# Kernel tuning notes

Hardware: AMD Instinct MI355X
Metric: run time of the kernel (lower is better)

## Reference

```python
import jax, jax.numpy as jnp
import numpy as np

CLAMP = 6.0  # clamp_delta


def _causal_dw_conv(x, w, b):
    # x: [B, D, L], w: [D, W] depthwise taps, b: [D]; torch Conv1d(groups=D, padding=W-1)[..., :L]
    W = w.shape[1]
    L = x.shape[-1]
    xp = jnp.pad(x, ((0, 0), (0, 0), (W - 1, 0)))
    y = b[None, :, None]
    for i in range(W):  # small fixed kernel width (2 or 4)
        y = y + xp[:, :, i:i + L] * w[:, i][None, :, None]
    return y


def _selective_scan(u, delta, A, Bm, Cm, D, z, delta_bias):
    # u, delta: [B, Di, L]; A: [Di, N]; Bm, Cm: [B, N, L]; D, delta_bias: [Di]; z: [B, Di, L]
    d = jax.nn.softplus(delta + delta_bias[None, :, None])

    def step(s, inp):
        d_t, b_t, c_t, u_t = inp  # [B,Di], [B,N], [B,N], [B,Di]
        s = s * jnp.exp(d_t[..., None] * A) + (d_t * u_t)[..., None] * b_t[:, None, :]
        return s, jnp.einsum('bdn,bn->bd', s, c_t)

    s0 = jnp.zeros((u.shape[0], A.shape[0], A.shape[1]), u.dtype)
    xs = (d.transpose(2, 0, 1), Bm.transpose(2, 0, 1), Cm.transpose(2, 0, 1), u.transpose(2, 0, 1))
    _, ys = jax.lax.scan(step, s0, xs)  # ys: [L, B, Di]
    y = ys.transpose(1, 2, 0) + D[:, None] * u
    return y * jax.nn.silu(z)


def _mamba(h, in_w, conv_w, conv_b, xproj_w, dt_w, dt_b, A_log, D, out_w):
    # standard Mamba block (no fast path), expand=1: h [B, L, dm] -> [B, L, dm]
    xz = jnp.einsum('bld,ed->bel', h, in_w)
    x, z = jnp.split(xz, 2, axis=1)
    x = jax.nn.silu(_causal_dw_conv(x, conv_w, conv_b))
    xdbl = jnp.einsum('bdl,ed->ble', x, xproj_w)
    r = dt_w.shape[1]
    n = A_log.shape[1]
    dt, Bm, Cm = jnp.split(xdbl, [r, r + n], axis=-1)
    delta = jnp.einsum('blr,dr->bdl', dt, dt_w)  # bias added inside scan as delta_bias
    y = _selective_scan(x, delta, -jnp.exp(A_log), Bm.transpose(0, 2, 1), Cm.transpose(0, 2, 1), D, z, dt_b)
    return jnp.einsum('bdl,ed->ble', y, out_w)


def setup_inputs() -> dict:
    rng = np.random.default_rng(0)
    dm, ds, dc, di, r = 1024, 16, 4, 2048, 64  # d_model, d_state, d_conv, d_inner, dt_rank
    mdm, mds, mdc, mr = 64, 4, 2, 4            # inner dt-Mamba dims (expand=1)
    B, L = 2, 1024

    def g(*s, std=0.02):
        return jnp.asarray(rng.standard_normal(s).astype(np.float32) * std)

    def inv_dt(d, lo=1e-3, hi=0.1):
        dt = np.exp(rng.uniform(size=d) * (np.log(hi) - np.log(lo)) + np.log(lo)).clip(min=1e-4)
        return jnp.asarray((dt + np.log(-np.expm1(-dt))).astype(np.float32))

    return dict(
        hidden_states=g(B, L, dm, std=1.0),
        in_proj_w=g(2 * di, dm),
        conv_w=g(di, dc, std=0.2),
        conv_b=g(di, std=0.02),
        x_proj_w=g(r + 2 * ds, di),
        dt_out_w=g(di, r, std=0.01),
        dt_out_b=inv_dt(di),
        A_log=jnp.log(jnp.tile(jnp.arange(1, ds + 1, dtype=jnp.float32), (di, 1))),
        D=jnp.ones(di, jnp.float32),
        out_proj_w=g(dm, di),
        m_in_w=g(2 * mdm, mdm),
        m_conv_w=g(mdm, mdc, std=0.3),
        m_conv_b=g(mdm, std=0.02),
        m_xproj_w=g(mr + 2 * mds, mdm),
        m_dt_w=g(mdm, mr, std=0.5),
        m_dt_b=inv_dt(mdm),
        m_A_log=jnp.log(jnp.tile(jnp.arange(1, mds + 1, dtype=jnp.float32), (mdm, 1))),
        m_D=jnp.ones(mdm, jnp.float32),
        m_out_w=g(mdm, mdm),
    )


def reference(hidden_states, in_proj_w, conv_w, conv_b, x_proj_w, dt_out_w, dt_out_b,
              A_log, D, out_proj_w, m_in_w, m_conv_w, m_conv_b, m_xproj_w, m_dt_w,
              m_dt_b, m_A_log, m_D, m_out_w):
    r = m_in_w.shape[1]  # dt_rank == inner d_model
    n = A_log.shape[1]   # d_state
    # in_proj (no bias): [B, 2*Di, L]
    xz = jnp.einsum('bld,ed->bel', hidden_states, in_proj_w)
    x, z = jnp.split(xz, 2, axis=1)
    x = jax.nn.silu(_causal_dw_conv(x, conv_w, conv_b))
    xdbl = jnp.einsum('bdl,ed->ble', x, x_proj_w)  # [B, L, r + 2n]
    dt_in, Bm, Cm = jnp.split(xdbl, [r, r + n], axis=-1)
    # nested dt-Mamba computes delta
    dt_m = _mamba(dt_in, m_in_w, m_conv_w, m_conv_b, m_xproj_w, m_dt_w, m_dt_b, m_A_log, m_D, m_out_w)
    delta = jnp.einsum('blr,dr->bld', dt_m, dt_out_w) + dt_out_b
    delta = jnp.clip(delta, -CLAMP, CLAMP).transpose(0, 2, 1)  # [B, Di, L]
    y = _selective_scan(x, delta, -jnp.exp(A_log), Bm.transpose(0, 2, 1), Cm.transpose(0, 2, 1),
                        D, z, dt_out_b)
    return jnp.einsum('bdl,ed->ble', y, out_proj_w)
```

## Files before the change

### kernel.cpp

```cpp
#include <hip/hip_runtime.h>
#include <hip/hip_bf16.h>

#define DEVFN __device__ __forceinline__

DEVFN float siluf(float x)     { return x / (1.f + __expf(-x)); }
DEVFN float softplusf(float x) { return fmaxf(x, 0.f) + log1pf(__expf(-fabsf(x))); }

DEVFN ushort f2bf(float f) {
    union { float f; unsigned u; } v; v.f = f;
    unsigned r = (v.u + 0x7FFF + ((v.u >> 16) & 1)) >> 16;
    return (ushort)r;
}

template<int CTRL>
DEVFN float dpp_addf(float x) {
    union { float f; int i; } a, r;
    a.f = x;
    r.i = __builtin_amdgcn_update_dpp(0, a.i, CTRL, 0xF, 0xF, true);
    return x + r.f;
}
DEVFN float sum16(float p) {
    p = dpp_addf<0x128>(p);
    p = dpp_addf<0x124>(p);
    p = dpp_addf<0x4E>(p);
    p = dpp_addf<0xB1>(p);
    return p;
}
DEVFN float sum4(float p) {
    p = dpp_addf<0x4E>(p);
    p = dpp_addf<0xB1>(p);
    return p;
}

typedef __bf16 bf16x8 __attribute__((ext_vector_type(8)));
typedef float  f32x4  __attribute__((ext_vector_type(4)));
typedef ushort us8    __attribute__((ext_vector_type(8)));

template<int BN, bool A_F32, bool B_F32>
__global__ __launch_bounds__(256) void mfma_gemm_nt(
    const void* __restrict__ Av, const void* __restrict__ Bv,
    float* __restrict__ C, int M, int N, int K,
    long long Abs, long long Bbs, long long Cbs)
{
    constexpr int BM = 128;
    constexpr int NFR = BN / 32;
    __shared__ __align__(16) ushort As[BM][40];
    __shared__ __align__(16) ushort Bs[BN][40];

    const int tid = threadIdx.x;
    const int m0 = blockIdx.x * BM;
    const int n0 = blockIdx.y * BN;
    const int b  = blockIdx.z;
    const int lane = tid & 63;
    const int wid  = tid >> 6;
    const int wr   = wid >> 1;
    const int wc   = wid & 1;
    const int fr   = lane & 15;
    const int kq   = lane >> 4;

    f32x4 acc[4][NFR];
    #pragma unroll
    for (int i = 0; i < 4; ++i)
        #pragma unroll
        for (int j = 0; j < NFR; ++j)
            acc[i][j] = (f32x4){0.f, 0.f, 0.f, 0.f};

    const int arow = tid >> 1;
    const int kh   = (tid & 1) * 16;

    for (int kt = 0; kt < K; kt += 32) {
        if (kt) __syncthreads();
        {
            const long long off = (long long)b * Abs + (long long)(m0 + arow) * K + kt + kh;
            us8 lo, hi;
            if (A_F32) {
                const float4* p = (const float4*)((const float*)Av + off);
                float4 v0 = p[0], v1 = p[1], v2 = p[2], v3 = p[3];
                lo = (us8){f2bf(v0.x), f2bf(v0.y), f2bf(v0.z), f2bf(v0.w),
                           f2bf(v1.x), f2bf(v1.y), f2bf(v1.z), f2bf(v1.w)};
                hi = (us8){f2bf(v2.x), f2bf(v2.y), f2bf(v2.z), f2bf(v2.w),
                           f2bf(v3.x), f2bf(v3.y), f2bf(v3.z), f2bf(v3.w)};
            } else {
                const us8* p = (const us8*)((const ushort*)Av + off);
                lo = p[0]; hi = p[1];
            }
            *(us8*)&As[arow][kh]     = lo;
            *(us8*)&As[arow][kh + 8] = hi;
        }
        if (BN == BM || arow < BN) {
            const long long off = (long long)b * Bbs + (long long)(n0 + arow) * K + kt + kh;
            us8 lo, hi;
            if (B_F32) {
                const float4* p = (const float4*)((const float*)Bv + off);
                float4 v0 = p[0], v1 = p[1], v2 = p[2], v3 = p[3];
                lo = (us8){f2bf(v0.x), f2bf(v0.y), f2bf(v0.z), f2bf(v0.w),
                           f2bf(v1.x), f2bf(v1.y), f2bf(v1.z), f2bf(v1.w)};
                hi = (us8){f2bf(v2.x), f2bf(v2.y), f2bf(v2.z), f2bf(v2.w),
                           f2bf(v3.x), f2bf(v3.y), f2bf(v3.z), f2bf(v3.w)};
            } else {
                const us8* p = (const us8*)((const ushort*)Bv + off);
                lo = p[0]; hi = p[1];
            }
            *(us8*)&Bs[arow][kh]     = lo;
            *(us8*)&Bs[arow][kh + 8] = hi;
        }
        __syncthreads();

        bf16x8 af[4], bfv[NFR];
        #pragma unroll
        for (int mi = 0; mi < 4; ++mi)
            af[mi] = *(const bf16x8*)&As[wr * 64 + mi * 16 + fr][kq * 8];
        #pragma unroll
        for (int ni = 0; ni < NFR; ++ni)
            bfv[ni] = *(const bf16x8*)&Bs[wc * (BN / 2) + ni * 16 + fr][kq * 8];
        #pragma unroll
        for (int mi = 0; mi < 4; ++mi)
            #pragma unroll
            for (int ni = 0; ni < NFR; ++ni)
                acc[mi][ni] = __builtin_amdgcn_mfma_f32_16x16x32_bf16(
                    af[mi], bfv[ni], acc[mi][ni], 0, 0, 0);
    }

    #pragma unroll
    for (int mi = 0; mi < 4; ++mi) {
        const int gm = m0 + wr * 64 + mi * 16 + kq * 4;
        #pragma unroll
        for (int ni = 0; ni < NFR; ++ni) {
            const int gn = n0 + wc * (BN / 2) + ni * 16 + fr;
            f32x4 v = acc[mi][ni];
            #pragma unroll
            for (int r = 0; r < 4; ++r)
                C[(long long)b * Cbs + (long long)(gm + r) * N + gn] = v[r];
        }
    }
}

__global__ __launch_bounds__(256) void transpose_f32_bf16(
    const float* __restrict__ y, ushort* __restrict__ yt,
    int D, int Lx, long long Ybs)
{
    __shared__ float ts[32][33];
    const int l0 = blockIdx.x * 32, d0 = blockIdx.y * 32, b = blockIdx.z;
    const int tx = threadIdx.x & 31, ty = threadIdx.x >> 5;
    const float* yb = y + (size_t)b * Ybs + (size_t)d0 * Lx + l0;
    #pragma unroll
    for (int r = ty; r < 32; r += 8)
        ts[r][tx] = yb[(size_t)r * Lx + tx];
    __syncthreads();
    ushort* ytb = yt + ((size_t)b * Lx + l0) * D + d0;
    #pragma unroll
    for (int r = ty; r < 32; r += 8)
        ytb[(size_t)r * D + tx] = f2bf(ts[tx][r]);
}

template<bool BKC, bool OUTM, bool CLIP, bool BIAS>
__global__ __launch_bounds__(256) void gemm_kernel(
    const float* __restrict__ A, const float* __restrict__ X,
    const float* __restrict__ bias, float* __restrict__ C,
    int M, int N, int K, int Xld, long long Xbs, long long Cbs)
{
    __shared__ __align__(16) float As[16][68];
    __shared__ __align__(16) float Xs[16][68];
    const int m0 = blockIdx.x * 64;
    const int n0 = blockIdx.y * 64;
    const int b  = blockIdx.z;
    const float* Xb = X + (long long)b * Xbs;
    const int tid = threadIdx.x;
    const int te = tid & 15, tl = tid >> 4;
    float acc[4][4] = {};

    for (int k0 = 0; k0 < K; k0 += 16) {
        #pragma unroll
        for (int idx = tid; idx < 1024; idx += 256) {
            int e = idx >> 4, kk = idx & 15;
            int m = m0 + e, k = k0 + kk;
            As[kk][e] = (m < M && k < K) ? A[(long long)m * K + k] : 0.f;
        }
        if (BKC) {
            #pragma unroll
            for (int idx = tid; idx < 1024; idx += 256) {
                int n = idx >> 4, kk = idx & 15;
                int nn = n0 + n, k = k0 + kk;
                Xs[kk][n] = (nn < N && k < K) ? Xb[(long long)nn * Xld + k] : 0.f;
            }
        } else {
            #pragma unroll
            for (int idx = tid; idx < 1024; idx += 256) {
                int kk = idx >> 6, n = idx & 63;
                int nn = n0 + n, k = k0 + kk;
                Xs[kk][n] = (nn < N && k < K) ? Xb[(long long)k * Xld + nn] : 0.f;
            }
        }
        __syncthreads();
        #pragma unroll
        for (int kk = 0; kk < 16; ++kk) {
            float4 a4 = *reinterpret_cast<const float4*>(&As[kk][te * 4]);
            float4 x4 = *reinterpret_cast<const float4*>(&Xs[kk][tl * 4]);
            float av[4] = {a4.x, a4.y, a4.z, a4.w};
            float xv[4] = {x4.x, x4.y, x4.z, x4.w};
            #pragma unroll
            for (int i = 0; i < 4; ++i)
                #pragma unroll
                for (int j = 0; j < 4; ++j)
                    acc[i][j] += av[i] * xv[j];
        }
        __syncthreads();
    }

    #pragma unroll
    for (int i = 0; i < 4; ++i) {
        int m = m0 + te * 4 + i;
        if (m >= M) continue;
        float bv = BIAS ? bias[m] : 0.f;
        #pragma unroll
        for (int j = 0; j < 4; ++j) {
            int n = n0 + tl * 4 + j;
            if (n >= N) continue;
            float v = acc[i][j] + bv;
            if (CLIP) v = fminf(fmaxf(v, -6.f), 6.f);
            if (OUTM) C[(long long)b * Cbs + (long long)m * N + n] = v;
            else      C[(long long)b * Cbs + (long long)n * M + m] = v;
        }
    }
}

__global__ __launch_bounds__(256) void xprojT_splitk(
    const float* __restrict__ W, const float* __restrict__ X,
    float* __restrict__ P, int L, int K, int KS)
{
    __shared__ float Xs[16][68];
    __shared__ float Ws[16][100];
    const int l0 = blockIdx.x * 64;
    const int ks = blockIdx.y;
    const int b  = blockIdx.z;
    const int Kc = K / KS;
    const int tid = threadIdx.x;
    const int tl = (tid & 15) * 4;
    const int te = (tid >> 4) * 6;
    float acc[4][6] = {};
    const float* Xb = X + (size_t)b * K * L;

    for (int d0 = ks * Kc; d0 < (ks + 1) * Kc; d0 += 16) {
        #pragma unroll
        for (int o = tid; o < 1024; o += 256) {
            int dd = o >> 6, l = o & 63;
            Xs[dd][l] = Xb[(size_t)(d0 + dd) * L + l0 + l];
        }
        #pragma unroll
        for (int o = tid; o < 1536; o += 256) {
            int e = o >> 4, dd = o & 15;
            Ws[dd][e] = W[(size_t)e * K + d0 + dd];
        }
        __syncthreads();
        #pragma unroll
        for (int dd = 0; dd < 16; ++dd) {
            float4 x4 = *(const float4*)&Xs[dd][tl];
            float xv[4] = {x4.x, x4.y, x4.z, x4.w};
            float wv[6];
            #pragma unroll
            for (int j = 0; j < 6; ++j) wv[j] = Ws[dd][te + j];
            #pragma unroll
            for (int i = 0; i < 4; ++i)
                #pragma unroll
                for (int j = 0; j < 6; ++j)
                    acc[i][j] += xv[i] * wv[j];
        }
        __syncthreads();
    }

    float* Pz = P + ((size_t)(b * KS + ks) * L + l0) * 96;
    #pragma unroll
    for (int i = 0; i < 4; ++i)
        #pragma unroll
        for (int j = 0; j < 6; ++j)
            Pz[(size_t)(tl + i) * 96 + te + j] = acc[i][j];
}

__global__ __launch_bounds__(256) void reduce_splitk(
    const float* __restrict__ P, float* __restrict__ C, int slab, int KS)
{
    const int i4 = blockIdx.x * 256 + threadIdx.x;
    const int b  = blockIdx.y;
    if (i4 * 4 >= slab) return;
    const float* base = P + (size_t)b * KS * slab + (size_t)i4 * 4;
    float4 acc = make_float4(0.f, 0.f, 0.f, 0.f);
    for (int ks = 0; ks < KS; ++ks) {
        float4 v = *(const float4*)(base + (size_t)ks * slab);
        acc.x += v.x; acc.y += v.y; acc.z += v.z; acc.w += v.w;
    }
    *(float4*)(C + (size_t)b * slab + (size_t)i4 * 4) = acc;
}

__global__ __launch_bounds__(256) void conv4_silu_kernel(
    const float* __restrict__ in, const float* __restrict__ w,
    const float* __restrict__ bias, float* __restrict__ out,
    int B, int D, int L, int IC)
{
    int idx = blockIdx.x * 256 + threadIdx.x;
    int nL4 = L >> 2;
    if (idx >= B * D * nL4) return;
    int l4 = (idx % nL4) * 4;
    int d  = (idx / nL4) % D;
    int b  = idx / (nL4 * D);
    const float* xp = in + ((size_t)b * IC + d) * L;
    float4 cur = *(const float4*)(xp + l4);
    float4 prev = make_float4(0.f, 0.f, 0.f, 0.f);
    if (l4) prev = *(const float4*)(xp + l4 - 4);
    const float4 wv = *(const float4*)(w + d * 4);
    float bv = bias[d];
    float y0 = bv + wv.x*prev.y + wv.y*prev.z + wv.z*prev.w + wv.w*cur.x;
    float y1 = bv + wv.x*prev.z + wv.y*prev.w + wv.z*cur.x  + wv.w*cur.y;
    float y2 = bv + wv.x*prev.w + wv.y*cur.x  + wv.z*cur.y  + wv.w*cur.z;
    float y3 = bv + wv.x*cur.x  + wv.y*cur.y  + wv.z*cur.z  + wv.w*cur.w;
    *(float4*)(out + ((size_t)b * D + d) * L + l4) =
        make_float4(siluf(y0), siluf(y1), siluf(y2), siluf(y3));
}

__global__ __launch_bounds__(256) void conv_silu_kernel(
    const float* __restrict__ in, const float* __restrict__ w,
    const float* __restrict__ bias, float* __restrict__ out,
    int B, int D, int L, int W, int IC)
{
    int idx = blockIdx.x * 256 + threadIdx.x;
    int total = B * D * L;
    if (idx >= total) return;
    int l = idx % L;
    int d = (idx / L) % D;
    int b = idx / (L * D);
    const float* xp = in + (size_t)b * IC * L + (size_t)d * L;
    float acc = bias[d];
    for (int i = 0; i < W; ++i) {
        int li = l - (W - 1) + i;
        if (li >= 0) acc += w[d * W + i] * xp[li];
    }
    out[(size_t)b * D * L + (size_t)d * L + l] = siluf(acc);
}

__global__ __launch_bounds__(256) void inner_xproj_dt_kernel(
    const float* __restrict__ mxconv, const float* __restrict__ xw,
    const float* __restrict__ dtw, float* __restrict__ mxdblT,
    float* __restrict__ mdelta, int L)
{
    __shared__ float xs[64][65];
    __shared__ float xwl[12][64];
    __shared__ float dtl[64][4];
    __shared__ float xd[4][65];
    const int tid = threadIdx.x;
    const int l0 = blockIdx.x * 64;
    const int b  = blockIdx.y;

    for (int o = tid; o < 4096; o += 256) {
        int k = o >> 6, l = o & 63;
        xs[k][l] = mxconv[((size_t)b * 64 + k) * L + l0 + l];
    }
    if (tid < 768) xwl[tid >> 6][tid & 63] = xw[tid];
    dtl[tid >> 2][tid & 3] = dtw[tid];
    __syncthreads();

    for (int o = tid; o < 768; o += 256) {
        int e = o >> 6, l = o & 63;
        float acc = 0.f;
        #pragma unroll
        for (int k = 0; k < 64; ++k) acc += xwl[e][k] * xs[k][l];
        mxdblT[((size_t)b * L + l0 + l) * 12 + e] = acc;
        if (e < 4) xd[e][l] = acc;
    }
    __syncthreads();

    for (int o = tid; o < 4096; o += 256) {
        int dch = o >> 6, l = o & 63;
        float acc = dtl[dch][0] * xd[0][l] + dtl[dch][1] * xd[1][l]
                  + dtl[dch][2] * xd[2][l] + dtl[dch][3] * xd[3][l];
        mdelta[((size_t)b * 64 + dch) * L + l0 + l] = acc;
    }
}

__global__ __launch_bounds__(256) void scan_outer4_kernel(
    const float* __restrict__ delta, const float* __restrict__ u,
    const float* __restrict__ xz, const float* __restrict__ xdblT,
    const float* __restrict__ A_log, const float* __restrict__ Dp,
    const float* __restrict__ dt_bias, float* __restrict__ y,
    int Dch, int L, long long Ybs)
{
    __shared__ float2 dtdu[16][66];
    __shared__ float2 PS[16][17];

    const int tid = threadIdx.x;
    const int b = blockIdx.y;
    const int d = blockIdx.x;
    const size_t rbase = ((size_t)b * Dch + d) * L;

    {
        const int l0 = tid * 4;
        float4 d4 = *(const float4*)(delta + rbase + l0);
        float4 u4 = *(const float4*)(u + rbase + l0);
        float bias = dt_bias[d];
        float dv[4] = {d4.x, d4.y, d4.z, d4.w};
        float uv[4] = {u4.x, u4.y, u4.z, u4.w};
        #pragma unroll
        for (int t = 0; t < 4; ++t) {
            float dt = softplusf(dv[t] + bias);
            dtdu[tid >> 4][(tid & 15) * 4 + t] = make_float2(dt, dt * uv[t]);
        }
    }
    __syncthreads();

    const int c = tid >> 4;
    const int n = tid & 15;
    const float Adn = -__expf(A_log[d * 16 + n]);
    const float* brow = xdblT + ((size_t)b * L + (size_t)c * 64) * 96 + 64 + n;

    float s = 0.f, sumdt = 0.f;
    for (int q = 0; q < 16; ++q) {
        #pragma unroll
        for (int t = 0; t < 4; ++t) {
            int l = q * 4 + t;
            float bv = brow[(size_t)l * 96];
            float2 dd = dtdu[c][l];
            float a = __expf(dd.x * Adn);
            s = fmaf(a, s, dd.y * bv);
            sumdt += dd.x;
        }
    }
    PS[n][c] = make_float2(__expf(sumdt * Adn), s);
    __syncthreads();

    float s0 = 0.f;
    for (int j = 0; j < c; ++j) {
        float2 ps = PS[n][j];
        s0 = fmaf(ps.x, s0, ps.y);
    }

    {
        const size_t ybase = (size_t)b * Ybs + (size_t)d * L + (size_t)c * 64;
        const float* up = u + rbase + (size_t)c * 64;
        const float* zp = xz + ((size_t)b * 2 * Dch + Dch + d) * L + c * 64;
        const float Dd = Dp[d];
        float s2 = s0;
        for (int q = 0; q < 16; ++q) {
            float4 u4 = *(const float4*)(up + q * 4);
            float4 z4 = *(const float4*)(zp + q * 4);
            float uv[4] = {u4.x, u4.y, u4.z, u4.w};
            float zv[4] = {z4.x, z4.y, z4.z, z4.w};
            float yv[4];
            #pragma unroll
            for (int t = 0; t < 4; ++t) {
                int l = q * 4 + t;
                float bv = brow[(size_t)l * 96];
                float cv = brow[(size_t)l * 96 + 16];
                float2 dd = dtdu[c][l];
                float a = __expf(dd.x * Adn);
                s2 = fmaf(a, s2, dd.y * bv);
                float p = sum16(s2 * cv);
                yv[t] = (p + Dd * uv[t]) * siluf(zv[t]);
            }
            if (n == 0)
                *(float4*)(y + ybase + q * 4) = make_float4(yv[0], yv[1], yv[2], yv[3]);
        }
    }
}

__global__ __launch_bounds__(256) void scan_inner4_kernel(
    const float* __restrict__ mdelta, const float* __restrict__ mu,
    const float* __restrict__ mxz, const float* __restrict__ mxdblT,
    const float* __restrict__ mA_log, const float* __restrict__ mDp,
    const float* __restrict__ mdt_b, float* __restrict__ ym, int L)
{
    __shared__ float2 dtdu[64][17];
    __shared__ float2 PS[4][66];

    const int tid = threadIdx.x;
    const int b = blockIdx.y;
    const int d = blockIdx.x;
    const size_t base = ((size_t)b * 64 + d) * L;

    {
        const int l0 = tid * 4;
        float4 d4 = *(const float4*)(mdelta + base + l0);
        float4 u4 = *(const float4*)(mu + base + l0);
        float bias = mdt_b[d];
        float dv[4] = {d4.x, d4.y, d4.z, d4.w};
        float uv[4] = {u4.x, u4.y, u4.z, u4.w};
        #pragma unroll
        for (int t = 0; t < 4; ++t) {
            float dt = softplusf(dv[t] + bias);
            dtdu[tid >> 2][(tid & 3) * 4 + t] = make_float2(dt, dt * uv[t]);
        }
    }
    __syncthreads();

    const int c = tid >> 2;
    const int n = tid & 3;
    const float Adn = -__expf(mA_log[d * 4 + n]);
    const float* brow = mxdblT + ((size_t)b * L + (size_t)c * 16) * 12 + 4 + n;

    float s = 0.f, sumdt = 0.f;
    for (int l = 0; l < 16; ++l) {
        float bv = brow[(size_t)l * 12];
        float2 dd = dtdu[c][l];
        float a = __expf(dd.x * Adn);
        s = fmaf(a, s, dd.y * bv);
        sumdt += dd.x;
    }
    PS[n][c] = make_float2(__expf(sumdt * Adn), s);
    __syncthreads();

    float s0 = 0.f;
    for (int j = 0; j < c; ++j) {
        float2 ps = PS[n][j];
        s0 = fmaf(ps.x, s0, ps.y);
    }

    {
        const float* up = mu + base + c * 16;
        const float* zp = mxz + ((size_t)b * 128 + 64 + d) * L + c * 16;
        const float Dd = mDp[d];
        float s2 = s0;
        for (int q = 0; q < 4; ++q) {
            float4 u4 = *(const float4*)(up + q * 4);
            float4 z4 = *(const float4*)(zp + q * 4);
            float uv[4] = {u4.x, u4.y, u4.z, u4.w};
            float zv[4] = {z4.x, z4.y, z4.z, z4.w};
            float yv[4];
            #pragma unroll
            for (int t = 0; t < 4; ++t) {
                int l = q * 4 + t;
                float bv = brow[(size_t)l * 12];
                float cv = brow[(size_t)l * 12 + 4];
                float2 dd = dtdu[c][l];
                float a = __expf(dd.x * Adn);
                s2 = fmaf(a, s2, dd.y * bv);
                float p = sum4(s2 * cv);
                yv[t] = (p + Dd * uv[t]) * siluf(zv[t]);
            }
            if (n == 0)
                *(float4*)(ym + base + c * 16 + q * 4) = make_float4(yv[0], yv[1], yv[2], yv[3]);
        }
    }
}

extern "C" void kernel_launch(void* const* d_in, const int* in_sizes, int n_in,
                              void* d_out, int out_size, void* d_ws, size_t ws_size,
                              hipStream_t stream)
{
    const float* h         = (const float*)d_in[0];
    const float* in_w      = (const float*)d_in[1];
    const float* conv_w    = (const float*)d_in[2];
    const float* conv_b    = (const float*)d_in[3];
    const float* xproj_w   = (const float*)d_in[4];
    const float* dt_out_w  = (const float*)d_in[5];
    const float* dt_out_b  = (const float*)d_in[6];
    const float* A_log     = (const float*)d_in[7];
    const float* Dp        = (const float*)d_in[8];
    const float* out_w     = (const float*)d_in[9];
    const float* m_in_w    = (const float*)d_in[10];
    const float* m_conv_w  = (const float*)d_in[11];
    const float* m_conv_b  = (const float*)d_in[12];
    const float* m_xproj_w = (const float*)d_in[13];
    const float* m_dt_w    = (const float*)d_in[14];
    const float* m_dt_b    = (const float*)d_in[15];
    const float* m_A_log   = (const float*)d_in[16];
    const float* m_Dp      = (const float*)d_in[17];
    const float* m_out_w   = (const float*)d_in[18];
    float* out = (float*)d_out;

    const int B = 2, L = 1024, dm = 1024, di = 2048;

    float* ws     = (float*)d_ws;
    float* xz     = ws;
    float* xconv  = xz     + (size_t)B * 2 * di * L;
    float* xdblT  = xconv  + (size_t)B * di * L;
    float* mxz    = xdblT  + (size_t)B * 96 * L;
    float* mxconv = mxz    + (size_t)B * 128 * L;
    float* mxdblT = mxconv + (size_t)B * 64 * L;
    float* mdelta = mxdblT + (size_t)B * 12 * L;
    float* ym     = mdelta + (size_t)B * 64 * L;
    float* dtm    = ym     + (size_t)B * 64 * L;
    float* delta  = dtm    + (size_t)B * 64 * L;
    ushort* yt    = (ushort*)delta;
    float* part   = delta;

    dim3 blk(256);

    mfma_gemm_nt<128, true, true><<<dim3(4096 / 128, L / 128, B), blk, 0, stream>>>(
        in_w, h, xz, 2 * di, L, dm, 0LL, (long long)L * dm, (long long)2 * di * L);

    {
        int total = B * di * (L / 4);
        conv4_silu_kernel<<<dim3((total + 255) / 256), blk, 0, stream>>>(
            xz, conv_w, conv_b, xconv, B, di, L, 2 * di);
    }

    {
        const int KS = 16;
        xprojT_splitk<<<dim3(L / 64, KS, B), blk, 0, stream>>>(
            xproj_w, xconv, part, L, di, KS);
        int slab = 96 * L;
        reduce_splitk<<<dim3((slab / 4 + 255) / 256, B), blk, 0, stream>>>(
            part, xdblT, slab, KS);
    }

    gemm_kernel<true, true, false, false><<<dim3(2, 16, B), blk, 0, stream>>>(
        m_in_w, xdblT, nullptr, mxz, 128, L, 64, 96, (long long)96 * L, (long long)128 * L);

    {
        int total = B * 64 * L;
        conv_silu_kernel<<<dim3((total + 255) / 256), blk, 0, stream>>>(
            mxz, m_conv_w, m_conv_b, mxconv, B, 64, L, 2, 128);
    }

    inner_xproj_dt_kernel<<<dim3(L / 64, B), blk, 0, stream>>>(
        mxconv, m_xproj_w, m_dt_w, mxdblT, mdelta, L);

    scan_inner4_kernel<<<dim3(64, B), blk, 0, stream>>>(
        mdelta, mxconv, mxz, mxdblT, m_A_log, m_Dp, m_dt_b, ym, L);

    gemm_kernel<false, true, false, false><<<dim3(1, 16, B), blk, 0, stream>>>(
        m_out_w, ym, nullptr, dtm, 64, L, 64, L, (long long)64 * L, (long long)64 * L);

    gemm_kernel<false, true, true, true><<<dim3(32, 16, B), blk, 0, stream>>>(
        dt_out_w, dtm, dt_out_b, delta, di, L, 64, L, (long long)64 * L, (long long)di * L);

    scan_outer4_kernel<<<dim3(di, B), blk, 0, stream>>>(
        delta, xconv, xz, xdblT, A_log, Dp, dt_out_b, xz, di, L, (long long)2 * di * L);

    transpose_f32_bf16<<<dim3(L / 32, di / 32, B), blk, 0, stream>>>(
        xz, yt, di, L, (long long)2 * di * L);

    mfma_gemm_nt<64, false, true><<<dim3(B * L / 128, dm / 64, 1), blk, 0, stream>>>(
        yt, out_w, out, B * L, dm, di, 0LL, 0LL, 0LL);
}
```

Baseline: 295.7 us.

## Fuse inner conv into xproj kernel and fuse inner out_proj with dt projection

Moves the inner depthwise conv+SiLU into the inner x_proj/dt kernel, which now reads mxz directly and writes mxconv as a side output. Also merges the inner out_proj GEMM and the dt_out projection (with bias and clamp) into one kernel that recomputes the 64x64 dtm tile per output block in shared memory. This removes two launches and the dtm round trip through global memory, at the cost of recomputing the small out_proj once for each of the 32 di-blocks.

New measurement: 293.1 us. No clear change (-0.9%).

```diff
diff --git a/kernel.cpp b/kernel.cpp
--- a/kernel.cpp
+++ b/kernel.cpp
@@ -316,30 +316,11 @@
         make_float4(siluf(y0), siluf(y1), siluf(y2), siluf(y3));
 }
 
-__global__ __launch_bounds__(256) void conv_silu_kernel(
-    const float* __restrict__ in, const float* __restrict__ w,
-    const float* __restrict__ bias, float* __restrict__ out,
-    int B, int D, int L, int W, int IC)
-{
-    int idx = blockIdx.x * 256 + threadIdx.x;
-    int total = B * D * L;
-    if (idx >= total) return;
-    int l = idx % L;
-    int d = (idx / L) % D;
-    int b = idx / (L * D);
-    const float* xp = in + (size_t)b * IC * L + (size_t)d * L;
-    float acc = bias[d];
-    for (int i = 0; i < W; ++i) {
-        int li = l - (W - 1) + i;
-        if (li >= 0) acc += w[d * W + i] * xp[li];
-    }
-    out[(size_t)b * D * L + (size_t)d * L + l] = siluf(acc);
-}
-
-__global__ __launch_bounds__(256) void inner_xproj_dt_kernel(
-    const float* __restrict__ mxconv, const float* __restrict__ xw,
-    const float* __restrict__ dtw, float* __restrict__ mxdblT,
-    float* __restrict__ mdelta, int L)
+__global__ __launch_bounds__(256) void inner_xproj_dt_conv_kernel(
+    const float* __restrict__ mxz, const float* __restrict__ cw,
+    const float* __restrict__ cb, const float* __restrict__ xw,
+    const float* __restrict__ dtw, float* __restrict__ mxconv,
+    float* __restrict__ mxdblT, float* __restrict__ mdelta, int L)
 {
     __shared__ float xs[64][65];
     __shared__ float xwl[12][64];
@@ -349,11 +330,32 @@
     const int l0 = blockIdx.x * 64;
     const int b  = blockIdx.y;
 
-    for (int o = tid; o < 4096; o += 256) {
-        int k = o >> 6, l = o & 63;
-        xs[k][l] = mxconv[((size_t)b * 64 + k) * L + l0 + l];
-    }
-    if (tid < 768) xwl[tid >> 6][tid & 63] = xw[tid];
+    {
+        const int k = tid >> 2, seg = (tid & 3) * 16;
+        const float* xp = mxz + ((size_t)b * 128 + k) * L + l0 + seg;
+        float prevv = (l0 + seg > 0) ? xp[-1] : 0.f;
+        float4 v0 = *(const float4*)(xp);
+        float4 v1 = *(const float4*)(xp + 4);
+        float4 v2 = *(const float4*)(xp + 8);
+        float4 v3 = *(const float4*)(xp + 12);
+        float vals[16] = {v0.x, v0.y, v0.z, v0.w, v1.x, v1.y, v1.z, v1.w,
+                          v2.x, v2.y, v2.z, v2.w, v3.x, v3.y, v3.z, v3.w};
+        const float w0 = cw[k * 2], w1 = cw[k * 2 + 1], bv = cb[k];
+        float outv[16];
+        #pragma unroll
+        for (int t = 0; t < 16; ++t) {
+            outv[t] = siluf(w0 * prevv + w1 * vals[t] + bv);
+            prevv = vals[t];
+        }
+        #pragma unroll
+        for (int t = 0; t < 16; ++t) xs[k][seg + t] = outv[t];
+        float* op = mxconv + ((size_t)b * 64 + k) * L + l0 + seg;
+        *(float4*)(op)      = make_float4(outv[0], outv[1], outv[2], outv[3]);
+        *(float4*)(op + 4)  = make_float4(outv[4], outv[5], outv[6], outv[7]);
+        *(float4*)(op + 8)  = make_float4(outv[8], outv[9], outv[10], outv[11]);
+        *(float4*)(op + 12) = make_float4(outv[12], outv[13], outv[14], outv[15]);
+    }
+    if (tid < 768) xwl[tid / 64][tid % 64] = xw[tid];
     dtl[tid >> 2][tid & 3] = dtw[tid];
     __syncthreads();
 
@@ -372,6 +374,70 @@
         float acc = dtl[dch][0] * xd[0][l] + dtl[dch][1] * xd[1][l]
                   + dtl[dch][2] * xd[2][l] + dtl[dch][3] * xd[3][l];
         mdelta[((size_t)b * 64 + dch) * L + l0 + l] = acc;
+    }
+}
+
+__global__ __launch_bounds__(256) void outproj_dt_kernel(
+    const float* __restrict__ ym, const float* __restrict__ mow,
+    const float* __restrict__ dtw, const float* __restrict__ dtb,
+    float* __restrict__ delta, int L, int Dch)
+{
+    __shared__ float xs[64][68];
+    __shared__ float ws[64][64];
+    __shared__ float dts[64][68];
+    __shared__ float As[16][68];
+    const int tid = threadIdx.x;
+    const int l0 = blockIdx.x * 64;
+    const int m0 = blockIdx.y * 64;
+    const int b  = blockIdx.z;
+
+    for (int o = tid; o < 4096; o += 256) {
+        int k = o >> 6, l = o & 63;
+        xs[k][l] = ym[((size_t)b * 64 + k) * L + l0 + l];
+        ws[k][l] = mow[o];
+    }
+    __syncthreads();
+
+    for (int o = tid; o < 4096; o += 256) {
+        int e = o >> 6, l = o & 63;
+        float acc = 0.f;
+        #pragma unroll
+        for (int k = 0; k < 64; ++k) acc += ws[e][k] * xs[k][l];
+        dts[e][l] = acc;
+    }
+
+    const int te = tid & 15, tl = tid >> 4;
+    float acc[4][4] = {};
+    for (int k0 = 0; k0 < 64; k0 += 16) {
+        __syncthreads();
+        for (int idx = tid; idx < 1024; idx += 256) {
+            int e = idx >> 6, m = idx & 63;
+            As[e][m] = dtw[(size_t)(m0 + m) * 64 + k0 + e];
+        }
+        __syncthreads();
+        #pragma unroll
+        for (int kk = 0; kk < 16; ++kk) {
+            float4 a4 = *(const float4*)&As[kk][te * 4];
+            float4 x4 = *(const float4*)&dts[k0 + kk][tl * 4];
+            float av[4] = {a4.x, a4.y, a4.z, a4.w};
+            float xv[4] = {x4.x, x4.y, x4.z, x4.w};
+            #pragma unroll
+            for (int i = 0; i < 4; ++i)
+                #pragma unroll
+                for (int j = 0; j < 4; ++j)
+                    acc[i][j] += av[i] * xv[j];
+        }
+    }
+
+    #pragma unroll
+    for (int i = 0; i < 4; ++i) {
+        int m = m0 + te * 4 + i;
+        float bv = dtb[m];
+        #pragma unroll
+        for (int j = 0; j < 4; ++j) {
+            float v = fminf(fmaxf(acc[i][j] + bv, -6.f), 6.f);
+            delta[((size_t)b * Dch + m) * L + l0 + tl * 4 + j] = v;
+        }
     }
 }
 
@@ -603,23 +669,14 @@
     gemm_kernel<true, true, false, false><<<dim3(2, 16, B), blk, 0, stream>>>(
         m_in_w, xdblT, nullptr, mxz, 128, L, 64, 96, (long long)96 * L, (long long)128 * L);
 
-    {
-        int total = B * 64 * L;
-        conv_silu_kernel<<<dim3((total + 255) / 256), blk, 0, stream>>>(
-            mxz, m_conv_w, m_conv_b, mxconv, B, 64, L, 2, 128);
-    }
-
-    inner_xproj_dt_kernel<<<dim3(L / 64, B), blk, 0, stream>>>(
-        mxconv, m_xproj_w, m_dt_w, mxdblT, mdelta, L);
+    inner_xproj_dt_conv_kernel<<<dim3(L / 64, B), blk, 0, stream>>>(
+        mxz, m_conv_w, m_conv_b, m_xproj_w, m_dt_w, mxconv, mxdblT, mdelta, L);
 
     scan_inner4_kernel<<<dim3(64, B), blk, 0, stream>>>(
         mdelta, mxconv, mxz, mxdblT, m_A_log, m_Dp, m_dt_b, ym, L);
 
-    gemm_kernel<false, true, false, false><<<dim3(1, 16, B), blk, 0, stream>>>(
-        m_out_w, ym, nullptr, dtm, 64, L, 64, L, (long long)64 * L, (long long)64 * L);
-
-    gemm_kernel<false, true, true, true><<<dim3(32, 16, B), blk, 0, stream>>>(
-        dt_out_w, dtm, dt_out_b, delta, di, L, 64, L, (long long)64 * L, (long long)di * L);
+    outproj_dt_kernel<<<dim3(L / 64, di / 64, B), blk, 0, stream>>>(
+        ym, m_out_w, dt_out_w, dt_out_b, delta, L, di);
 
     scan_outer4_kernel<<<dim3(di, B), blk, 0, stream>>>(
         delta, xconv, xz, xdblT, A_log, Dp, dt_out_b, xz, di, L, (long long)2 * di * L);
```
